# Kernel tuning notes

Measured on AMD Instinct MI355X. Metric: run time of the kernel, lower is better.

Reference implementation:

```python
import jax, jax.numpy as jnp
import numpy as np

N, T, C, H = 32, 512, 768, 1536  # batch, seq_len, dim, int(dim*expand)


def setup_inputs() -> dict:
    key = jax.random.key(0)
    ks = jax.random.split(key, 10)
    sc = lambda fan: 1.0 / np.sqrt(fan)
    return {
        "x_seq": jax.random.normal(ks[0], (N, T, C), jnp.float32),
        "sup_seq": jax.random.uniform(ks[1], (N, T, 1), jnp.float32),
        # torch nn.Linear weights are [out, in]; y = x @ W.T + b
        "W_in": jax.random.normal(ks[2], (C, C), jnp.float32) * sc(C),
        "W_out": jax.random.normal(ks[3], (C, C), jnp.float32) * sc(C),
        "W_bg": jax.random.normal(ks[4], (C, C), jnp.float32) * sc(C),
        "b_bg": jax.random.normal(ks[5], (C,), jnp.float32) * 0.01,
        "W_sg": jax.random.normal(ks[6], (C, 1), jnp.float32),
        "b_sg": jax.random.normal(ks[7], (C,), jnp.float32) * 0.01,
        "W_f1": jax.random.normal(ks[8], (H, C), jnp.float32) * sc(C),
        "b_f1": jnp.zeros((H,), jnp.float32),
        "W_f2": jax.random.normal(ks[9], (C, H), jnp.float32) * sc(H),
        "b_f2": jnp.zeros((C,), jnp.float32),
    }


def reference(x_seq, sup_seq, W_in, W_out, W_bg, b_bg, W_sg, b_sg, W_f1, b_f1, W_f2, b_f2):
    # in_proj (no bias)
    x = jnp.einsum('ntc,dc->ntd', x_seq, W_in)                      # [N,T,C]
    # per-step FFN with residual (exact erf GELU, matching torch default)
    h = jax.nn.gelu(jnp.einsum('ntc,hc->nth', x, W_f1) + b_f1, approximate=False)
    xt = x + jnp.einsum('nth,ch->ntc', h, W_f2) + b_f2              # [N,T,C]
    # input-dependent gate (base_gate * sup_to_gate)
    g = jax.nn.sigmoid(jnp.einsum('ntc,dc->ntd', xt, W_bg) + b_bg)
    g = g * jax.nn.sigmoid(jnp.einsum('nto,do->ntd', sup_seq, W_sg) + b_sg)
    # linear recurrence s_t = (1-g_t)*s_{t-1} + g_t*xt_t, s_0 = 0 -> associative scan
    a = 1.0 - g
    b = g * xt

    def combine(c1, c2):
        a1, b1 = c1
        a2, b2 = c2
        return a2 * a1, a2 * b1 + b2

    _, s = jax.lax.associative_scan(combine, (a, b), axis=1)        # [N,T,C]
    return jnp.einsum('ntc,dc->ntd', s, W_out)
```

## Files before the change

### kernel.cpp

```cpp
#include <hip/hip_runtime.h>
#include <hip/hip_bf16.h>
#include <math.h>

typedef __bf16 bf16;
typedef __attribute__((ext_vector_type(8))) __bf16 bf16x8;
typedef __attribute__((ext_vector_type(4))) __bf16 bf16x4;
typedef __attribute__((ext_vector_type(4))) float f32x4;

constexpr int BM = 128, BN = 128, BK = 32;
constexpr int LDK = BK + 24;

enum { EPI_PLAIN = 0, EPI_GELU = 1, EPI_RES = 2, EPI_GATE = 3 };

template <typename AT, typename CT, int EPI>
__global__ __launch_bounds__(256, 2) void gemm_bt(
    const AT* __restrict__ A, const bf16* __restrict__ B, CT* __restrict__ C,
    const float* __restrict__ bias, const float* __restrict__ resid,
    const float* __restrict__ sup, const float* __restrict__ wsg,
    const float* __restrict__ bsg, int M, int N, int K) {
  __shared__ bf16 As[BM][LDK];
  __shared__ bf16 Bs[BN][LDK];

  const int tid = threadIdx.x;
  const int bm = blockIdx.x, bn = blockIdx.y;
  const int lane = tid & 63;
  const int w = tid >> 6;
  const int wm = (w >> 1) * 64, wn = (w & 1) * 64;
  const int quad = lane >> 4, l16 = lane & 15;

  f32x4 acc[4][4];
#pragma unroll
  for (int i = 0; i < 4; i++)
#pragma unroll
    for (int j = 0; j < 4; j++) acc[i][j] = f32x4{0.f, 0.f, 0.f, 0.f};

  const AT* Ab = A + (size_t)(bm * BM) * K;
  const bf16* Bb = B + (size_t)(bn * BN) * K;

  for (int kk = 0; kk < K; kk += BK) {
    if constexpr (sizeof(AT) == 4) {
#pragma unroll
      for (int it = 0; it < 4; ++it) {
        int id = it * 256 + tid;
        int row = id >> 3, k4 = id & 7;
        f32x4 v = *(const f32x4*)((const float*)Ab + (size_t)row * K + kk + k4 * 4);
        bf16x4 b;
        b[0] = (bf16)v[0]; b[1] = (bf16)v[1]; b[2] = (bf16)v[2]; b[3] = (bf16)v[3];
        *(bf16x4*)&As[row][k4 * 4] = b;
      }
    } else {
#pragma unroll
      for (int it = 0; it < 2; ++it) {
        int id = it * 256 + tid;
        int row = id >> 2, k8 = id & 3;
        bf16x8 v = *(const bf16x8*)((const bf16*)Ab + (size_t)row * K + kk + k8 * 8);
        *(bf16x8*)&As[row][k8 * 8] = v;
      }
    }
#pragma unroll
    for (int it = 0; it < 2; ++it) {
      int id = it * 256 + tid;
      int row = id >> 2, k8 = id & 3;
      bf16x8 v = *(const bf16x8*)(Bb + (size_t)row * K + kk + k8 * 8);
      *(bf16x8*)&Bs[row][k8 * 8] = v;
    }
    __syncthreads();

    bf16x8 af[4], bfr[4];
#pragma unroll
    for (int i = 0; i < 4; i++) af[i] = *(const bf16x8*)&As[wm + i * 16 + l16][quad * 8];
#pragma unroll
    for (int j = 0; j < 4; j++) bfr[j] = *(const bf16x8*)&Bs[wn + j * 16 + l16][quad * 8];
#pragma unroll
    for (int i = 0; i < 4; i++)
#pragma unroll
      for (int j = 0; j < 4; j++)
        acc[i][j] = __builtin_amdgcn_mfma_f32_16x16x32_bf16(af[i], bfr[j], acc[i][j], 0, 0, 0);
    __syncthreads();
  }

#pragma unroll
  for (int i = 0; i < 4; i++) {
    int row0 = bm * BM + wm + i * 16 + quad * 4;
#pragma unroll
    for (int j = 0; j < 4; j++) {
      int col = bn * BN + wn + j * 16 + l16;
#pragma unroll
      for (int r = 0; r < 4; r++) {
        int row = row0 + r;
        size_t idx = (size_t)row * N + col;
        float v = acc[i][j][r];
        if constexpr (EPI == EPI_PLAIN) {
          C[idx] = (CT)v;
        } else if constexpr (EPI == EPI_GELU) {
          v += bias[col];
          float gl = 0.5f * v * (1.0f + erff(v * 0.70710678118654752f));
          C[idx] = (CT)gl;
        } else if constexpr (EPI == EPI_RES) {
          v += bias[col] + resid[idx];
          C[idx] = (CT)v;
        } else {
          v += bias[col];
          float g1 = 1.0f / (1.0f + expf(-v));
          float z = sup[row] * wsg[col] + bsg[col];
          float g2 = 1.0f / (1.0f + expf(-z));
          C[idx] = (CT)(g1 * g2);
        }
      }
    }
  }
}

constexpr int SC_CH = 32;
constexpr int SC_NCH = 16;
constexpr int SC_CW = 32;

__global__ __launch_bounds__(512) void scan2_kernel(const float* __restrict__ g,
                                                    const float* __restrict__ xt,
                                                    bf16* __restrict__ s, int T, int C) {
  __shared__ float lA[SC_NCH][SC_CW];
  __shared__ float lB[SC_NCH][SC_CW];
  __shared__ float lC[SC_NCH][SC_CW];
  const int cl = threadIdx.x & (SC_CW - 1);
  const int ch = threadIdx.x / SC_CW;
  const int c = blockIdx.x * SC_CW + cl;
  const int n = blockIdx.y;
  const size_t base = ((size_t)n * T + ch * SC_CH) * C + c;

  float a_arr[SC_CH], sl[SC_CH];
  float A = 1.f, B = 0.f;
#pragma unroll
  for (int t = 0; t < SC_CH; ++t) {
    size_t idx = base + (size_t)t * C;
    float gv = g[idx], xv = xt[idx];
    float at = 1.0f - gv;
    a_arr[t] = at;
    B = at * B + gv * xv;
    sl[t] = B;
    A *= at;
  }
  lA[ch][cl] = A;
  lB[ch][cl] = B;
  __syncthreads();
  if (ch == 0) {
    float carry = 0.f;
#pragma unroll
    for (int j = 0; j < SC_NCH; ++j) {
      lC[j][cl] = carry;
      carry = lA[j][cl] * carry + lB[j][cl];
    }
  }
  __syncthreads();
  const float carry = lC[ch][cl];
  float P = 1.f;
#pragma unroll
  for (int t = 0; t < SC_CH; ++t) {
    P *= a_arr[t];
    s[base + (size_t)t * C] = (bf16)(sl[t] + P * carry);
  }
}

__global__ __launch_bounds__(256) void cvt_kernel(const float* __restrict__ in,
                                                  bf16* __restrict__ out, int n) {
  int i = blockIdx.x * 256 + threadIdx.x;
  if (i < n) out[i] = (bf16)in[i];
}

extern "C" void kernel_launch(void* const* d_in, const int* in_sizes, int n_in,
                              void* d_out, int out_size, void* d_ws, size_t ws_size,
                              hipStream_t stream) {
  const float* x_seq = (const float*)d_in[0];
  const float* sup = (const float*)d_in[1];
  const float* W_in = (const float*)d_in[2];
  const float* W_out = (const float*)d_in[3];
  const float* W_bg = (const float*)d_in[4];
  const float* b_bg = (const float*)d_in[5];
  const float* W_sg = (const float*)d_in[6];
  const float* b_sg = (const float*)d_in[7];
  const float* W_f1 = (const float*)d_in[8];
  const float* b_f1 = (const float*)d_in[9];
  const float* W_f2 = (const float*)d_in[10];
  const float* b_f2 = (const float*)d_in[11];

  const int Nb = 32, T = 512, C = 768, H = 1536;
  const int M = Nb * T;

  char* ws = (char*)d_ws;
  size_t off = 0;
  auto alloc = [&](size_t bytes) {
    void* p = ws + off;
    off += (bytes + 255) & ~(size_t)255;
    return p;
  };
  bf16* Win_bf = (bf16*)alloc((size_t)C * C * 2);
  bf16* Wf1_bf = (bf16*)alloc((size_t)H * C * 2);
  bf16* Wf2_bf = (bf16*)alloc((size_t)C * H * 2);
  bf16* Wbg_bf = (bf16*)alloc((size_t)C * C * 2);
  bf16* Wout_bf = (bf16*)alloc((size_t)C * C * 2);
  float* x_f = (float*)alloc((size_t)M * C * 4);
  bf16* h_bf = (bf16*)alloc((size_t)M * H * 2);
  float* xt_f = (float*)alloc((size_t)M * C * 4);
  float* g_f = (float*)alloc((size_t)M * C * 4);
  bf16* s_bf = (bf16*)x_f;

  auto cvt = [&](const float* src, bf16* dst, int n) {
    cvt_kernel<<<(n + 255) / 256, 256, 0, stream>>>(src, dst, n);
  };
  cvt(W_in, Win_bf, C * C);
  cvt(W_f1, Wf1_bf, H * C);
  cvt(W_f2, Wf2_bf, C * H);
  cvt(W_bg, Wbg_bf, C * C);
  cvt(W_out, Wout_bf, C * C);

  dim3 blk(256);
  gemm_bt<float, float, EPI_PLAIN><<<dim3(M / BM, C / BN), blk, 0, stream>>>(
      x_seq, Win_bf, x_f, nullptr, nullptr, nullptr, nullptr, nullptr, M, C, C);
  gemm_bt<float, bf16, EPI_GELU><<<dim3(M / BM, H / BN), blk, 0, stream>>>(
      x_f, Wf1_bf, h_bf, b_f1, nullptr, nullptr, nullptr, nullptr, M, H, C);
  gemm_bt<bf16, float, EPI_RES><<<dim3(M / BM, C / BN), blk, 0, stream>>>(
      h_bf, Wf2_bf, xt_f, b_f2, x_f, nullptr, nullptr, nullptr, M, C, H);
  gemm_bt<float, float, EPI_GATE><<<dim3(M / BM, C / BN), blk, 0, stream>>>(
      xt_f, Wbg_bf, g_f, b_bg, nullptr, sup, W_sg, b_sg, M, C, C);
  scan2_kernel<<<dim3(C / SC_CW, Nb), dim3(SC_CW * SC_NCH), 0, stream>>>(
      g_f, xt_f, s_bf, T, C);
  gemm_bt<bf16, float, EPI_PLAIN><<<dim3(M / BM, C / BN), blk, 0, stream>>>(
      s_bf, Wout_bf, (float*)d_out, nullptr, nullptr, nullptr, nullptr, nullptr, M, C, C);
}
```

Measured before the change: 393.2 us.

## Store intermediates in bf16 and load GEMM tiles via global_load_lds

Intermediate activations x and xt are now stored as bf16 instead of fp32, halving their write and read traffic. GEMMs with bf16 A operands use direct global-to-LDS async loads into unpadded shared tiles instead of staging through registers. The five weight conversions are merged into a single launch. The changes risk LDS bank conflicts from the unpadded layout, and the residual and scan input lose precision.

```diff
diff --git a/kernel.cpp b/kernel.cpp
--- a/kernel.cpp
+++ b/kernel.cpp
@@ -12,20 +12,26 @@
 
 enum { EPI_PLAIN = 0, EPI_GELU = 1, EPI_RES = 2, EPI_GATE = 3 };
 
-template <typename AT, typename CT, int EPI>
-__global__ __launch_bounds__(256, 2) void gemm_bt(
-    const AT* __restrict__ A, const bf16* __restrict__ B, CT* __restrict__ C,
-    const float* __restrict__ bias, const float* __restrict__ resid,
+__device__ __forceinline__ void async16(const void* g, void* l) {
+  __builtin_amdgcn_global_load_lds(
+      (const __attribute__((address_space(1))) void*)g,
+      (__attribute__((address_space(3))) void*)l, 16, 0, 0);
+}
+
+template <typename CT, int EPI>
+__global__ __launch_bounds__(256, 2) void gemm_bt_a(
+    const bf16* __restrict__ A, const bf16* __restrict__ B, CT* __restrict__ C,
+    const float* __restrict__ bias, const bf16* __restrict__ resid,
     const float* __restrict__ sup, const float* __restrict__ wsg,
     const float* __restrict__ bsg, int M, int N, int K) {
-  __shared__ bf16 As[BM][LDK];
-  __shared__ bf16 Bs[BN][LDK];
+  __shared__ bf16 As[BM * BK];
+  __shared__ bf16 Bs[BN * BK];
 
   const int tid = threadIdx.x;
   const int bm = blockIdx.x, bn = blockIdx.y;
   const int lane = tid & 63;
-  const int w = tid >> 6;
-  const int wm = (w >> 1) * 64, wn = (w & 1) * 64;
+  const int wv = tid >> 6;
+  const int wm = (wv >> 1) * 64, wn = (wv & 1) * 64;
   const int quad = lane >> 4, l16 = lane & 15;
 
   f32x4 acc[4][4];
@@ -34,43 +40,28 @@
 #pragma unroll
     for (int j = 0; j < 4; j++) acc[i][j] = f32x4{0.f, 0.f, 0.f, 0.f};
 
-  const AT* Ab = A + (size_t)(bm * BM) * K;
+  const bf16* Ab = A + (size_t)(bm * BM) * K;
   const bf16* Bb = B + (size_t)(bn * BN) * K;
+  const int srow = tid >> 2, sk8 = (tid & 3) * 8;
 
   for (int kk = 0; kk < K; kk += BK) {
-    if constexpr (sizeof(AT) == 4) {
-#pragma unroll
-      for (int it = 0; it < 4; ++it) {
-        int id = it * 256 + tid;
-        int row = id >> 3, k4 = id & 7;
-        f32x4 v = *(const f32x4*)((const float*)Ab + (size_t)row * K + kk + k4 * 4);
-        bf16x4 b;
-        b[0] = (bf16)v[0]; b[1] = (bf16)v[1]; b[2] = (bf16)v[2]; b[3] = (bf16)v[3];
-        *(bf16x4*)&As[row][k4 * 4] = b;
-      }
-    } else {
-#pragma unroll
-      for (int it = 0; it < 2; ++it) {
-        int id = it * 256 + tid;
-        int row = id >> 2, k8 = id & 3;
-        bf16x8 v = *(const bf16x8*)((const bf16*)Ab + (size_t)row * K + kk + k8 * 8);
-        *(bf16x8*)&As[row][k8 * 8] = v;
-      }
-    }
-#pragma unroll
-    for (int it = 0; it < 2; ++it) {
-      int id = it * 256 + tid;
-      int row = id >> 2, k8 = id & 3;
-      bf16x8 v = *(const bf16x8*)(Bb + (size_t)row * K + kk + k8 * 8);
-      *(bf16x8*)&Bs[row][k8 * 8] = v;
+#pragma unroll
+    for (int it = 0; it < 4; ++it) {
+      int row = it * 64 + srow;
+      async16(Ab + (size_t)row * K + kk + sk8, &As[(it * 256 + wv * 64) * 8]);
+    }
+#pragma unroll
+    for (int it = 0; it < 4; ++it) {
+      int row = it * 64 + srow;
+      async16(Bb + (size_t)row * K + kk + sk8, &Bs[(it * 256 + wv * 64) * 8]);
     }
     __syncthreads();
 
     bf16x8 af[4], bfr[4];
 #pragma unroll
-    for (int i = 0; i < 4; i++) af[i] = *(const bf16x8*)&As[wm + i * 16 + l16][quad * 8];
-#pragma unroll
-    for (int j = 0; j < 4; j++) bfr[j] = *(const bf16x8*)&Bs[wn + j * 16 + l16][quad * 8];
+    for (int i = 0; i < 4; i++) af[i] = *(const bf16x8*)&As[(wm + i * 16 + l16) * BK + quad * 8];
+#pragma unroll
+    for (int j = 0; j < 4; j++) bfr[j] = *(const bf16x8*)&Bs[(wn + j * 16 + l16) * BK + quad * 8];
 #pragma unroll
     for (int i = 0; i < 4; i++)
 #pragma unroll
@@ -97,7 +88,7 @@
           float gl = 0.5f * v * (1.0f + erff(v * 0.70710678118654752f));
           C[idx] = (CT)gl;
         } else if constexpr (EPI == EPI_RES) {
-          v += bias[col] + resid[idx];
+          v += bias[col] + (float)resid[idx];
           C[idx] = (CT)v;
         } else {
           v += bias[col];
@@ -111,12 +102,80 @@
   }
 }
 
-constexpr int SC_CH = 32;
-constexpr int SC_NCH = 16;
-constexpr int SC_CW = 32;
+template <typename CT, int EPI>
+__global__ __launch_bounds__(256, 2) void gemm_bt_f(
+    const float* __restrict__ A, const bf16* __restrict__ B, CT* __restrict__ C,
+    const float* __restrict__ bias, int M, int N, int K) {
+  __shared__ bf16 As[BM][LDK];
+  __shared__ bf16 Bs[BN][LDK];
+
+  const int tid = threadIdx.x;
+  const int bm = blockIdx.x, bn = blockIdx.y;
+  const int lane = tid & 63;
+  const int wv = tid >> 6;
+  const int wm = (wv >> 1) * 64, wn = (wv & 1) * 64;
+  const int quad = lane >> 4, l16 = lane & 15;
+
+  f32x4 acc[4][4];
+#pragma unroll
+  for (int i = 0; i < 4; i++)
+#pragma unroll
+    for (int j = 0; j < 4; j++) acc[i][j] = f32x4{0.f, 0.f, 0.f, 0.f};
+
+  const float* Ab = A + (size_t)(bm * BM) * K;
+  const bf16* Bb = B + (size_t)(bn * BN) * K;
+
+  for (int kk = 0; kk < K; kk += BK) {
+#pragma unroll
+    for (int it = 0; it < 4; ++it) {
+      int id = it * 256 + tid;
+      int row = id >> 3, k4 = id & 7;
+      f32x4 v = *(const f32x4*)(Ab + (size_t)row * K + kk + k4 * 4);
+      bf16x4 b;
+      b[0] = (bf16)v[0]; b[1] = (bf16)v[1]; b[2] = (bf16)v[2]; b[3] = (bf16)v[3];
+      *(bf16x4*)&As[row][k4 * 4] = b;
+    }
+#pragma unroll
+    for (int it = 0; it < 2; ++it) {
+      int id = it * 256 + tid;
+      int row = id >> 2, k8 = id & 3;
+      bf16x8 v = *(const bf16x8*)(Bb + (size_t)row * K + kk + k8 * 8);
+      *(bf16x8*)&Bs[row][k8 * 8] = v;
+    }
+    __syncthreads();
+
+    bf16x8 af[4], bfr[4];
+#pragma unroll
+    for (int i = 0; i < 4; i++) af[i] = *(const bf16x8*)&As[wm + i * 16 + l16][quad * 8];
+#pragma unroll
+    for (int j = 0; j < 4; j++) bfr[j] = *(const bf16x8*)&Bs[wn + j * 16 + l16][quad * 8];
+#pragma unroll
+    for (int i = 0; i < 4; i++)
+#pragma unroll
+      for (int j = 0; j < 4; j++)
+        acc[i][j] = __builtin_amdgcn_mfma_f32_16x16x32_bf16(af[i], bfr[j], acc[i][j], 0, 0, 0);
+    __syncthreads();
+  }
+
+#pragma unroll
+  for (int i = 0; i < 4; i++) {
+    int row0 = bm * BM + wm + i * 16 + quad * 4;
+#pragma unroll
+    for (int j = 0; j < 4; j++) {
+      int col = bn * BN + wn + j * 16 + l16;
+#pragma unroll
+      for (int r = 0; r < 4; r++) {
+        size_t idx = (size_t)(row0 + r) * N + col;
+        C[idx] = (CT)acc[i][j][r];
+      }
+    }
+  }
+}
+
+constexpr int SC_CH = 32, SC_NCH = 16, SC_CW = 32;
 
 __global__ __launch_bounds__(512) void scan2_kernel(const float* __restrict__ g,
-                                                    const float* __restrict__ xt,
+                                                    const bf16* __restrict__ xt,
                                                     bf16* __restrict__ s, int T, int C) {
   __shared__ float lA[SC_NCH][SC_CW];
   __shared__ float lB[SC_NCH][SC_CW];
@@ -132,7 +191,7 @@
 #pragma unroll
   for (int t = 0; t < SC_CH; ++t) {
     size_t idx = base + (size_t)t * C;
-    float gv = g[idx], xv = xt[idx];
+    float gv = g[idx], xv = (float)xt[idx];
     float at = 1.0f - gv;
     a_arr[t] = at;
     B = at * B + gv * xv;
@@ -160,10 +219,20 @@
   }
 }
 
-__global__ __launch_bounds__(256) void cvt_kernel(const float* __restrict__ in,
-                                                  bf16* __restrict__ out, int n) {
+__global__ __launch_bounds__(256) void cvt5_kernel(
+    const float* s0, bf16* d0, int n0, const float* s1, bf16* d1, int n1,
+    const float* s2, bf16* d2, int n2, const float* s3, bf16* d3, int n3,
+    const float* s4, bf16* d4, int n4) {
+  const float* s; bf16* d; int n;
+  switch (blockIdx.y) {
+    case 0: s = s0; d = d0; n = n0; break;
+    case 1: s = s1; d = d1; n = n1; break;
+    case 2: s = s2; d = d2; n = n2; break;
+    case 3: s = s3; d = d3; n = n3; break;
+    default: s = s4; d = d4; n = n4; break;
+  }
   int i = blockIdx.x * 256 + threadIdx.x;
-  if (i < n) out[i] = (bf16)in[i];
+  if (i < n) d[i] = (bf16)s[i];
 }
 
 extern "C" void kernel_launch(void* const* d_in, const int* in_sizes, int n_in,
@@ -197,32 +266,27 @@
   bf16* Wf2_bf = (bf16*)alloc((size_t)C * H * 2);
   bf16* Wbg_bf = (bf16*)alloc((size_t)C * C * 2);
   bf16* Wout_bf = (bf16*)alloc((size_t)C * C * 2);
-  float* x_f = (float*)alloc((size_t)M * C * 4);
+  bf16* x_bf = (bf16*)alloc((size_t)M * C * 2);
   bf16* h_bf = (bf16*)alloc((size_t)M * H * 2);
-  float* xt_f = (float*)alloc((size_t)M * C * 4);
+  bf16* xt_bf = (bf16*)alloc((size_t)M * C * 2);
   float* g_f = (float*)alloc((size_t)M * C * 4);
-  bf16* s_bf = (bf16*)x_f;
-
-  auto cvt = [&](const float* src, bf16* dst, int n) {
-    cvt_kernel<<<(n + 255) / 256, 256, 0, stream>>>(src, dst, n);
-  };
-  cvt(W_in, Win_bf, C * C);
-  cvt(W_f1, Wf1_bf, H * C);
-  cvt(W_f2, Wf2_bf, C * H);
-  cvt(W_bg, Wbg_bf, C * C);
-  cvt(W_out, Wout_bf, C * C);
+  bf16* s_bf = x_bf;
+
+  cvt5_kernel<<<dim3((H * C + 255) / 256, 5), 256, 0, stream>>>(
+      W_in, Win_bf, C * C, W_f1, Wf1_bf, H * C, W_f2, Wf2_bf, C * H,
+      W_bg, Wbg_bf, C * C, W_out, Wout_bf, C * C);
 
   dim3 blk(256);
-  gemm_bt<float, float, EPI_PLAIN><<<dim3(M / BM, C / BN), blk, 0, stream>>>(
-      x_seq, Win_bf, x_f, nullptr, nullptr, nullptr, nullptr, nullptr, M, C, C);
-  gemm_bt<float, bf16, EPI_GELU><<<dim3(M / BM, H / BN), blk, 0, stream>>>(
-      x_f, Wf1_bf, h_bf, b_f1, nullptr, nullptr, nullptr, nullptr, M, H, C);
-  gemm_bt<bf16, float, EPI_RES><<<dim3(M / BM, C / BN), blk, 0, stream>>>(
-      h_bf, Wf2_bf, xt_f, b_f2, x_f, nullptr, nullptr, nullptr, M, C, H);
-  gemm_bt<float, float, EPI_GATE><<<dim3(M / BM, C / BN), blk, 0, stream>>>(
-      xt_f, Wbg_bf, g_f, b_bg, nullptr, sup, W_sg, b_sg, M, C, C);
+  gemm_bt_f<bf16, EPI_PLAIN><<<dim3(M / BM, C / BN), blk, 0, stream>>>(
+      x_seq, Win_bf, x_bf, nullptr, M, C, C);
+  gemm_bt_a<bf16, EPI_GELU><<<dim3(M / BM, H / BN), blk, 0, stream>>>(
+      x_bf, Wf1_bf, h_bf, b_f1, nullptr, nullptr, nullptr, nullptr, M, H, C);
+  gemm_bt_a<bf16, EPI_RES><<<dim3(M / BM, C / BN), blk, 0, stream>>>(
+      h_bf, Wf2_bf, xt_bf, b_f2, x_bf, nullptr, nullptr, nullptr, M, C, H);
+  gemm_bt_a<float, EPI_GATE><<<dim3(M / BM, C / BN), blk, 0, stream>>>(
+      xt_bf, Wbg_bf, g_f, b_bg, nullptr, sup, W_sg, b_sg, M, C, C);
   scan2_kernel<<<dim3(C / SC_CW, Nb), dim3(SC_CW * SC_NCH), 0, stream>>>(
-      g_f, xt_f, s_bf, T, C);
-  gemm_bt<bf16, float, EPI_PLAIN><<<dim3(M / BM, C / BN), blk, 0, stream>>>(
+      g_f, xt_bf, s_bf, T, C);
+  gemm_bt_a<float, EPI_PLAIN><<<dim3(M / BM, C / BN), blk, 0, stream>>>(
       s_bf, Wout_bf, (float*)d_out, nullptr, nullptr, nullptr, nullptr, nullptr, M, C, C);
 }
```

After: 441.8 us. +12.4%, slower.
